# Kernel optimization log

Hardware: AMD Instinct MI355X
Metric: run time of the kernel (lower is better)

Reference implementation:

```python
import jax, jax.numpy as jnp
import numpy as np


def setup_inputs() -> dict:
    key = jax.random.key(0)
    ks = jax.random.split(key, 7)
    B, T, IN_F = 16384, 64, 48
    F = 32          # feature_size = len(INTERACTIVE_LIST)
    H = 128         # embedding_hidden_size
    TF, TH = T * F, T * H
    scale1 = 1.0 / np.sqrt(TF)
    scale2 = 1.0 / np.sqrt(TH)
    return {
        "x": jax.random.normal(ks[0], (B, T, IN_F), dtype=jnp.float32),
        "W1": jax.random.normal(ks[1], (TF, TH), dtype=jnp.float32) * scale1,
        "b1": jax.random.normal(ks[2], (TH,), dtype=jnp.float32) * scale1,
        "W2": jax.random.normal(ks[3], (TH, TF), dtype=jnp.float32) * scale2,
        "b2": jax.random.normal(ks[4], (TF,), dtype=jnp.float32) * scale2,
        "weight": jax.random.normal(ks[5], (T, F), dtype=jnp.float32),
        "bias": jax.random.normal(ks[6], (F,), dtype=jnp.float32) * (1.0 / np.sqrt(T)),
        "sample_index": jnp.arange(F, dtype=jnp.int32),
    }


def reference(x, W1, b1, W2, b2, weight, bias, sample_index):
    # x: [B, T, IN_F]; gather interactive feature columns -> [B, T, F]
    B = x.shape[0]
    T, F = weight.shape
    xs = jnp.take(x, sample_index, axis=2)            # [B, T, F]
    # pass_linear=True path: MLP on flattened time*feature vector
    h = jax.nn.relu(xs.reshape(B, T * F) @ W1 + b1)   # [B, T*H]; dropout = identity (eval)
    out = (h @ W2 + b2).reshape(B, T, F)              # [B, T, F]
    # vectorized form of the per-sample loop: sum over time of elementwise mul
    emb = jnp.einsum("btf,tf->bf", out, weight) + bias  # [B, F]
    return emb
```

## Files before the change

### kernel.cpp

```cpp
#include <hip/hip_runtime.h>
#include <hip/hip_bf16.h>

#define BATCH 16384
#define TT    64
#define INF   48
#define FF    32
#define TFD   2048
#define THD   8192

typedef __attribute__((ext_vector_type(8))) short bf16x8;
typedef __attribute__((ext_vector_type(4))) short bf16x4;
typedef __attribute__((ext_vector_type(4))) short short4v;
typedef __attribute__((ext_vector_type(4))) float f32x4;

#define SCHED __builtin_amdgcn_sched_barrier(0)
#define VMW(n) asm volatile("s_waitcnt vmcnt(" #n ")" ::: "memory")

__device__ inline void gload_lds16(const void* g, void* l) {
  __builtin_amdgcn_global_load_lds((const __attribute__((address_space(1))) void*)g,
                                   (__attribute__((address_space(3))) void*)l, 16, 0, 0);
}

__device__ inline f32x4 mfma16x16x16_bf16(bf16x4 a, bf16x4 b, f32x4 c) {
#if __has_builtin(__builtin_amdgcn_mfma_f32_16x16x16bf16_1k)
  return __builtin_amdgcn_mfma_f32_16x16x16bf16_1k(a, b, c, 0, 0, 0);
#else
  asm("v_mfma_f32_16x16x16_bf16 %0, %1, %2, %0" : "+v"(c) : "v"(a), "v"(b));
  return c;
#endif
}

__device__ inline short f32_to_bf16_bits(float x) {
  __hip_bfloat16 h = __float2bfloat16(x);
  return *reinterpret_cast<short*>(&h);
}


__global__ void gather_cast_frag(const float* __restrict__ x, const int* __restrict__ sidx,
                                 __hip_bfloat16* __restrict__ xsf) {
  __shared__ int sx[FF];
  if (threadIdx.x < FF) sx[threadIdx.x] = sidx[threadIdx.x];
  __syncthreads();
  const int b64 = blockIdx.x >> 2;
  const int tq  = blockIdx.x & 3;
  for (int it = 0; it < 16; ++it) {
    const int slot = (tq * 16 + it) * 256 + threadIdx.x;
    const int t  = slot >> 8;
    const int bi = (slot >> 6) & 3;
    const int l  = slot & 63;
    const int lo = l & 15, hi = l >> 4;
    const int row = b64 * 64 + bi * 16 + lo;
    const float* rp = x + ((size_t)row * TT + t) * INF;
    bf16x8 v;
    #pragma unroll
    for (int j = 0; j < 8; ++j) v[j] = f32_to_bf16_bits(rp[sx[hi * 8 + j]]);
    *(bf16x8*)(xsf + ((size_t)b64 * 16384 + slot) * 8) = v;
  }
}

__global__ void transpose_w1(const float* __restrict__ W1, __hip_bfloat16* __restrict__ W1t) {
  __shared__ float tile[64][65];
  const int k0 = blockIdx.x * 64;
  const int n0 = blockIdx.y * 64;
  const int tx = threadIdx.x & 63, ty = threadIdx.x >> 6;
  for (int r = ty; r < 64; r += 4)
    tile[r][tx] = W1[(size_t)(k0 + r) * THD + n0 + tx];
  __syncthreads();
  const int rn = threadIdx.x >> 4;
  const int kq = (threadIdx.x & 15) * 4;
  for (int rr = rn; rr < 64; rr += 16) {
    short4v v;
    #pragma unroll
    for (int i = 0; i < 4; ++i) v[i] = f32_to_bf16_bits(tile[kq + i][rr]);
    *(short4v*)(W1t + (size_t)(n0 + rr) * TFD + k0 + kq) = v;
  }
}

__global__ void make_w2eff(const float* __restrict__ W2, const float* __restrict__ b2,
                           const float* __restrict__ weight, const float* __restrict__ bias,
                           __hip_bfloat16* __restrict__ w2t, float* __restrict__ beff) {
  const int n = blockIdx.x * 8 + (threadIdx.x >> 5);
  const int f = threadIdx.x & 31;
  const float* wr = W2 + (size_t)n * TFD;
  float s = 0.f;
  #pragma unroll 8
  for (int t = 0; t < TT; ++t) s += wr[t * FF + f] * weight[t * FF + f];
  w2t[(size_t)f * THD + n] = __float2bfloat16(s);
  if (blockIdx.x == 0 && threadIdx.x < FF) {
    float sb = bias[f];
    for (int t = 0; t < TT; ++t) sb += b2[t * FF + f] * weight[t * FF + f];
    beff[f] = sb;
  }
}


__device__ inline void stage_w(char* buf, const __hip_bfloat16* __restrict__ w1t,
                               int n0, int k0, int wid, int l) {
  const int sub = l >> 3;
  const int c   = (l & 7) ^ sub;
  const int h   = c >> 2, kc = c & 3;
  const int r0  = wid * 8 + sub;
  const __hip_bfloat16* gw0 = w1t + (size_t)(n0 + 2 * r0 + h) * TFD + k0 + kc * 8;
  const __hip_bfloat16* gw1 = w1t + (size_t)(n0 + 128 + 2 * r0 + h) * TFD + k0 + kc * 8;
  char* lx = buf + wid * 1024;
  gload_lds16(gw0, lx);
  gload_lds16(gw1, lx + 8192);
}

__device__ __forceinline__ void k_iter(char* lds, int v, int strip,
    const char* __restrict__ xbase, const __hip_bfloat16* __restrict__ w1t,
    f32x4 (&acc)[8][4], bf16x8 (&xfu)[4],
    int wbase, int wid, int l, bool do_bar) {
  if (v <= 252) {
    const int vs = v + 3;
    stage_w(lds + (size_t)(vs & 7) * 16384, w1t,
            strip * 1024 + (vs >> 6) * 256, (vs & 63) * 32, wid, l);
  }
  SCHED;
  const char* buf = lds + (size_t)(v & 7) * 16384;
  bf16x8 w0  = *(const bf16x8*)(buf + wbase);
  bf16x8 w1f = *(const bf16x8*)(buf + wbase + 1024);
  #pragma unroll
  for (int g = 0; g < 4; ++g) {
    bf16x8 nw0, nw1;
    if (g < 3) {
      nw0 = *(const bf16x8*)(buf + wbase + (2 * g + 2) * 1024);
      nw1 = *(const bf16x8*)(buf + wbase + (2 * g + 3) * 1024);
    }
    __builtin_amdgcn_s_setprio(1);
    #pragma unroll
    for (int bi = 0; bi < 4; ++bi)
      acc[2 * g][bi] = __builtin_amdgcn_mfma_f32_16x16x32_bf16(w0, xfu[bi], acc[2 * g][bi], 0, 0, 0);
    #pragma unroll
    for (int bi = 0; bi < 4; ++bi)
      acc[2 * g + 1][bi] = __builtin_amdgcn_mfma_f32_16x16x32_bf16(w1f, xfu[bi], acc[2 * g + 1][bi], 0, 0, 0);
    __builtin_amdgcn_s_setprio(0);
    if (g < 3) { w0 = nw0; w1f = nw1; }
  }
  if (v <= 253) {
    const int u = (v + 2) & 63;
    #pragma unroll
    for (int bi = 0; bi < 4; ++bi)
      xfu[bi] = *(const bf16x8*)(xbase + (u * 4 + bi) * 1024);
  }
  SCHED;
  if (v <= 252)      { VMW(6); }
  else if (v == 253) { VMW(4); }
  else               { VMW(0); }
  SCHED;
  if (do_bar) {
    __builtin_amdgcn_s_barrier(); SCHED;
  }
}

__global__ __launch_bounds__(512, 2) void gemm_fused(
    const __hip_bfloat16* __restrict__ xsf,
    const __hip_bfloat16* __restrict__ w1t,
    const float* __restrict__ b1,
    const __hip_bfloat16* __restrict__ w2t,
    float* __restrict__ partial)
{
  __shared__ __align__(16) char lds[131072];
  const int tid = threadIdx.x;
  const int wid = tid >> 6, l = tid & 63;
  const int mq = wid >> 2, bq = wid & 3;
  const int lo = l & 15, hi = l >> 4;
  const int rl = lo >> 1;
  const int cofs = (((((lo & 1) << 2) | hi) ^ rl) << 4);
  const int strip = blockIdx.x & 7;
  const int bt = blockIdx.x >> 3;
  const int b0 = bt * 256;

  const int wbase = ((mq << 6) + rl) * 128 + cofs;
  const char* xbase = (const char*)xsf + ((size_t)(bt * 4 + bq) * 16384 + l) * 16;

  f32x4 acc2[2][4];
  #pragma unroll
  for (int fi = 0; fi < 2; ++fi)
    #pragma unroll
    for (int bi = 0; bi < 4; ++bi) { f32x4 z = {0.f,0.f,0.f,0.f}; acc2[fi][bi] = z; }

  f32x4 acc[8][4];
  #pragma unroll
  for (int mi = 0; mi < 8; ++mi)
    #pragma unroll
    for (int bi = 0; bi < 4; ++bi) { f32x4 z = {0.f,0.f,0.f,0.f}; acc[mi][bi] = z; }

  bf16x8 xfA[4], xfB[4];
  stage_w(lds, w1t, strip * 1024, 0, wid, l);
  SCHED;
  #pragma unroll
  for (int bi = 0; bi < 4; ++bi) xfA[bi] = *(const bf16x8*)(xbase + (0 * 4 + bi) * 1024);
  SCHED;
  stage_w(lds + 16384, w1t, strip * 1024, 32, wid, l);
  SCHED;
  #pragma unroll
  for (int bi = 0; bi < 4; ++bi) xfB[bi] = *(const bf16x8*)(xbase + (1 * 4 + bi) * 1024);
  SCHED;
  stage_w(lds + 32768, w1t, strip * 1024, 64, wid, l);
  SCHED;
  VMW(8); SCHED;
  __builtin_amdgcn_s_barrier(); SCHED;

  for (int vv = 0; vv < 256; vv += 2) {
    k_iter(lds, vv,     strip, xbase, w1t, acc, xfA, wbase, wid, l, false);
    k_iter(lds, vv + 1, strip, xbase, w1t, acc, xfB, wbase, wid, l, true);

    if ((vv & 63) == 62) {
      const int n0e = strip * 1024 + (vv >> 6) * 256;
      #pragma unroll
      for (int mi = 0; mi < 8; ++mi) {
        const int nbase = n0e + (mq << 7) + (mi << 4);
        const float4 b1v = *(const float4*)(b1 + nbase + (hi << 2));
        bf16x4 p[4];
        #pragma unroll
        for (int bi = 0; bi < 4; ++bi) {
          bf16x4 pk;
          #pragma unroll
          for (int j = 0; j < 4; ++j) {
            float v = acc[mi][bi][j] + ((const float*)&b1v)[j];
            v = v > 0.f ? v : 0.f;
            pk[j] = f32_to_bf16_bits(v);
          }
          p[bi] = pk;
        }
        bf16x4 a2[2];
        #pragma unroll
        for (int fi = 0; fi < 2; ++fi)
          a2[fi] = *(const bf16x4*)(w2t + (size_t)(fi * 16 + lo) * THD + nbase + (hi << 2));
        #pragma unroll
        for (int fi = 0; fi < 2; ++fi)
          #pragma unroll
          for (int bi = 0; bi < 4; ++bi)
            acc2[fi][bi] = mfma16x16x16_bf16(a2[fi], p[bi], acc2[fi][bi]);
        #pragma unroll
        for (int bi = 0; bi < 4; ++bi) { f32x4 z = {0.f,0.f,0.f,0.f}; acc[mi][bi] = z; }
      }
    }
  }

  float* sm = (float*)lds;
  __syncthreads();
  if (mq == 1) {
    #pragma unroll
    for (int fi = 0; fi < 2; ++fi)
      #pragma unroll
      for (int bi = 0; bi < 4; ++bi)
        *(f32x4*)(sm + ((bq << 6) + (bi << 4) + lo) * 32 + fi * 16 + (hi << 2)) = acc2[fi][bi];
  }
  __syncthreads();
  if (mq == 0) {
    #pragma unroll
    for (int fi = 0; fi < 2; ++fi)
      #pragma unroll
      for (int bi = 0; bi < 4; ++bi) {
        f32x4 other = *(const f32x4*)(sm + ((bq << 6) + (bi << 4) + lo) * 32 + fi * 16 + (hi << 2));
        f32x4 v = acc2[fi][bi] + other;
        *(f32x4*)(partial + ((size_t)strip * BATCH + b0 + (bq << 6) + (bi << 4) + lo) * FF + fi * 16 + (hi << 2)) = v;
      }
  }
}

__global__ void reduce_partial(const float* __restrict__ partial, const float* __restrict__ beff,
                               float* __restrict__ out) {
  const int idx = blockIdx.x * 256 + threadIdx.x;
  float s = beff[idx & 31];
  #pragma unroll
  for (int c = 0; c < 8; ++c) s += partial[(size_t)c * BATCH * FF + idx];
  out[idx] = s;
}


extern "C" void kernel_launch(void* const* d_in, const int* in_sizes, int n_in,
                              void* d_out, int out_size, void* d_ws, size_t ws_size,
                              hipStream_t stream) {
  const float* x      = (const float*)d_in[0];
  const float* W1     = (const float*)d_in[1];
  const float* b1     = (const float*)d_in[2];
  const float* W2     = (const float*)d_in[3];
  const float* b2     = (const float*)d_in[4];
  const float* weight = (const float*)d_in[5];
  const float* bias   = (const float*)d_in[6];
  const int*   sidx   = (const int*)d_in[7];

  char* ws = (char*)d_ws;
  __hip_bfloat16* xsf  = (__hip_bfloat16*)ws;
  __hip_bfloat16* w1t  = (__hip_bfloat16*)(ws + 67108864);
  __hip_bfloat16* w2t  = (__hip_bfloat16*)(ws + 100663296);
  float*          beff = (float*)(ws + 101187584);
  float*          part = (float*)(ws + 101188608);

  hipLaunchKernelGGL(gather_cast_frag, dim3(1024), dim3(256), 0, stream, x, sidx, xsf);
  hipLaunchKernelGGL(transpose_w1, dim3(32, 128), dim3(256), 0, stream, W1, w1t);
  hipLaunchKernelGGL(make_w2eff,   dim3(1024),    dim3(256), 0, stream, W2, b2, weight, bias, w2t, beff);
  hipLaunchKernelGGL(gemm_fused,   dim3(512),     dim3(512), 0, stream, xsf, w1t, b1, w2t, part);
  hipLaunchKernelGGL(reduce_partial, dim3(2048),  dim3(256), 0, stream, part, beff, (float*)d_out);
}
```

Before: 597.4 us.

## Switch fused GEMM to 32x32x16 MFMA tiles with matching fragment layouts

Replaces the 16x16x32 bf16 MFMA tiling in the main GEMM with 32x32x16 MFMAs. This changes the x fragment layout produced by the gather kernel, the LDS staging and swizzle of W1, and the accumulator shapes. The second GEMM now also uses 32x32 MFMAs, with a per-lane LDS exchange to rebuild the B fragment from the accumulator layout. The aim is fewer MFMA and LDS-read instructions per flop and higher MFMA throughput. The cost is extra LDS round trips and waits in the epilogue, and larger accumulator register tiles.

```diff
diff --git a/kernel.cpp b/kernel.cpp
--- a/kernel.cpp
+++ b/kernel.cpp
@@ -9,30 +9,31 @@
 #define THD   8192
 
 typedef __attribute__((ext_vector_type(8))) short bf16x8;
-typedef __attribute__((ext_vector_type(4))) short bf16x4;
 typedef __attribute__((ext_vector_type(4))) short short4v;
 typedef __attribute__((ext_vector_type(4))) float f32x4;
+typedef __attribute__((ext_vector_type(16))) float f32x16;
 
 #define SCHED __builtin_amdgcn_sched_barrier(0)
 #define VMW(n) asm volatile("s_waitcnt vmcnt(" #n ")" ::: "memory")
+#define LGKM0  asm volatile("s_waitcnt lgkmcnt(0)" ::: "memory")
 
 __device__ inline void gload_lds16(const void* g, void* l) {
   __builtin_amdgcn_global_load_lds((const __attribute__((address_space(1))) void*)g,
                                    (__attribute__((address_space(3))) void*)l, 16, 0, 0);
 }
 
-__device__ inline f32x4 mfma16x16x16_bf16(bf16x4 a, bf16x4 b, f32x4 c) {
-#if __has_builtin(__builtin_amdgcn_mfma_f32_16x16x16bf16_1k)
-  return __builtin_amdgcn_mfma_f32_16x16x16bf16_1k(a, b, c, 0, 0, 0);
-#else
-  asm("v_mfma_f32_16x16x16_bf16 %0, %1, %2, %0" : "+v"(c) : "v"(a), "v"(b));
-  return c;
-#endif
+__device__ inline f32x16 mfma32(bf16x8 a, bf16x8 b, f32x16 c) {
+  return __builtin_amdgcn_mfma_f32_32x32x16_bf16(a, b, c, 0, 0, 0);
 }
 
 __device__ inline short f32_to_bf16_bits(float x) {
   __hip_bfloat16 h = __float2bfloat16(x);
   return *reinterpret_cast<short*>(&h);
+}
+
+__device__ inline unsigned packbf(float a, float b) {
+  return ((unsigned)(unsigned short)f32_to_bf16_bits(b) << 16) |
+         (unsigned)(unsigned short)f32_to_bf16_bits(a);
 }
 
 
@@ -41,20 +42,19 @@
   __shared__ int sx[FF];
   if (threadIdx.x < FF) sx[threadIdx.x] = sidx[threadIdx.x];
   __syncthreads();
-  const int b64 = blockIdx.x >> 2;
-  const int tq  = blockIdx.x & 3;
-  for (int it = 0; it < 16; ++it) {
-    const int slot = (tq * 16 + it) * 256 + threadIdx.x;
-    const int t  = slot >> 8;
-    const int bi = (slot >> 6) & 3;
-    const int l  = slot & 63;
-    const int lo = l & 15, hi = l >> 4;
-    const int row = b64 * 64 + bi * 16 + lo;
-    const float* rp = x + ((size_t)row * TT + t) * INF;
+  const int g32 = blockIdx.x;
+  for (int it = 0; it < 32; ++it) {
+    const int slot = it * 256 + threadIdx.x;
+    const int u16 = slot >> 6;
+    const int l   = slot & 63;
+    const int lo  = l & 31, hi = l >> 5;
+    const int t   = u16 >> 1;
+    const int fb  = ((u16 & 1) << 4) + (hi << 3);
+    const float* rp = x + ((size_t)(g32 * 32 + lo) * TT + t) * INF;
     bf16x8 v;
     #pragma unroll
-    for (int j = 0; j < 8; ++j) v[j] = f32_to_bf16_bits(rp[sx[hi * 8 + j]]);
-    *(bf16x8*)(xsf + ((size_t)b64 * 16384 + slot) * 8) = v;
+    for (int j = 0; j < 8; ++j) v[j] = f32_to_bf16_bits(rp[sx[fb + j]]);
+    *(bf16x8*)(xsf + ((size_t)g32 * 8192 + slot) * 8) = v;
   }
 }
 
@@ -94,54 +94,49 @@
 }
 
 
-__device__ inline void stage_w(char* buf, const __hip_bfloat16* __restrict__ w1t,
-                               int n0, int k0, int wid, int l) {
-  const int sub = l >> 3;
-  const int c   = (l & 7) ^ sub;
-  const int h   = c >> 2, kc = c & 3;
-  const int r0  = wid * 8 + sub;
-  const __hip_bfloat16* gw0 = w1t + (size_t)(n0 + 2 * r0 + h) * TFD + k0 + kc * 8;
-  const __hip_bfloat16* gw1 = w1t + (size_t)(n0 + 128 + 2 * r0 + h) * TFD + k0 + kc * 8;
-  char* lx = buf + wid * 1024;
-  gload_lds16(gw0, lx);
-  gload_lds16(gw1, lx + 8192);
+__device__ inline void stage_w32(char* buf, const __hip_bfloat16* __restrict__ w1t,
+                                 int n0, int k0, int wid, int l) {
+  const int e = l >> 3;
+  const int p = l & 7;
+  #pragma unroll
+  for (int j = 0; j < 2; ++j) {
+    const int q  = j * 8 + e;
+    const int c  = q * 8 + (p ^ e);
+    const int R  = c >> 2, kc = c & 3;
+    const __hip_bfloat16* g = w1t + (size_t)(n0 + wid * 32 + R) * TFD + k0 + kc * 8;
+    gload_lds16(g, buf + wid * 2048 + j * 1024);
+  }
 }
 
 __device__ __forceinline__ void k_iter(char* lds, int v, int strip,
-    const char* __restrict__ xbase, const __hip_bfloat16* __restrict__ w1t,
-    f32x4 (&acc)[8][4], bf16x8 (&xfu)[4],
-    int wbase, int wid, int l, bool do_bar) {
+    const char* __restrict__ xb0, const char* __restrict__ xb1,
+    const __hip_bfloat16* __restrict__ w1t,
+    f32x16 (&acc)[4][2], bf16x8 (&xfu)[4],
+    int gbase, int rdo0, int rdo1, int wid, int l, bool do_bar) {
   if (v <= 252) {
     const int vs = v + 3;
-    stage_w(lds + (size_t)(vs & 7) * 16384, w1t,
-            strip * 1024 + (vs >> 6) * 256, (vs & 63) * 32, wid, l);
-  }
-  SCHED;
-  const char* buf = lds + (size_t)(v & 7) * 16384;
-  bf16x8 w0  = *(const bf16x8*)(buf + wbase);
-  bf16x8 w1f = *(const bf16x8*)(buf + wbase + 1024);
+    stage_w32(lds + (size_t)(vs & 7) * 16384, w1t,
+              strip * 1024 + (vs >> 6) * 256, (vs & 63) * 32, wid, l);
+  }
+  SCHED;
+  const char* buf = lds + (size_t)(v & 7) * 16384 + gbase;
   #pragma unroll
-  for (int g = 0; g < 4; ++g) {
-    bf16x8 nw0, nw1;
-    if (g < 3) {
-      nw0 = *(const bf16x8*)(buf + wbase + (2 * g + 2) * 1024);
-      nw1 = *(const bf16x8*)(buf + wbase + (2 * g + 3) * 1024);
-    }
+  for (int nt = 0; nt < 4; ++nt) {
+    const bf16x8 w0  = *(const bf16x8*)(buf + nt * 2048 + rdo0);
+    const bf16x8 w1f = *(const bf16x8*)(buf + nt * 2048 + rdo1);
     __builtin_amdgcn_s_setprio(1);
-    #pragma unroll
-    for (int bi = 0; bi < 4; ++bi)
-      acc[2 * g][bi] = __builtin_amdgcn_mfma_f32_16x16x32_bf16(w0, xfu[bi], acc[2 * g][bi], 0, 0, 0);
-    #pragma unroll
-    for (int bi = 0; bi < 4; ++bi)
-      acc[2 * g + 1][bi] = __builtin_amdgcn_mfma_f32_16x16x32_bf16(w1f, xfu[bi], acc[2 * g + 1][bi], 0, 0, 0);
+    acc[nt][0] = mfma32(w0,  xfu[0], acc[nt][0]);
+    acc[nt][0] = mfma32(w1f, xfu[1], acc[nt][0]);
+    acc[nt][1] = mfma32(w0,  xfu[2], acc[nt][1]);
+    acc[nt][1] = mfma32(w1f, xfu[3], acc[nt][1]);
     __builtin_amdgcn_s_setprio(0);
-    if (g < 3) { w0 = nw0; w1f = nw1; }
   }
   if (v <= 253) {
     const int u = (v + 2) & 63;
-    #pragma unroll
-    for (int bi = 0; bi < 4; ++bi)
-      xfu[bi] = *(const bf16x8*)(xbase + (u * 4 + bi) * 1024);
+    xfu[0] = *(const bf16x8*)(xb0 + (u * 2 + 0) * 1024);
+    xfu[1] = *(const bf16x8*)(xb0 + (u * 2 + 1) * 1024);
+    xfu[2] = *(const bf16x8*)(xb1 + (u * 2 + 0) * 1024);
+    xfu[3] = *(const bf16x8*)(xb1 + (u * 2 + 1) * 1024);
   }
   SCHED;
   if (v <= 252)      { VMW(6); }
@@ -164,77 +159,91 @@
   const int tid = threadIdx.x;
   const int wid = tid >> 6, l = tid & 63;
   const int mq = wid >> 2, bq = wid & 3;
-  const int lo = l & 15, hi = l >> 4;
-  const int rl = lo >> 1;
-  const int cofs = (((((lo & 1) << 2) | hi) ^ rl) << 4);
+  const int lo = l & 31, hi = l >> 5;
   const int strip = blockIdx.x & 7;
   const int bt = blockIdx.x >> 3;
   const int b0 = bt * 256;
 
-  const int wbase = ((mq << 6) + rl) * 128 + cofs;
-  const char* xbase = (const char*)xsf + ((size_t)(bt * 4 + bq) * 16384 + l) * 16;
-
-  f32x4 acc2[2][4];
+  int rdo0, rdo1;
+  {
+    const int c0 = (lo << 2) + hi;       const int q0 = c0 >> 3;
+    rdo0 = (q0 << 7) + ((((c0 & 7) ^ (q0 & 7))) << 4);
+    const int c1 = c0 + 2;               const int q1 = c1 >> 3;
+    rdo1 = (q1 << 7) + ((((c1 & 7) ^ (q1 & 7))) << 4);
+  }
+  const int gbase = mq << 13;
+
+  const char* xb0 = (const char*)xsf + (size_t)(bt * 8 + bq * 2) * 131072 + l * 16;
+  const char* xb1 = xb0 + 131072;
+
+  const f32x16 vzero = {0.f,0.f,0.f,0.f,0.f,0.f,0.f,0.f,0.f,0.f,0.f,0.f,0.f,0.f,0.f,0.f};
+
+  f32x16 acc2[2];
+  acc2[0] = vzero; acc2[1] = vzero;
+
+  f32x16 acc[4][2];
   #pragma unroll
-  for (int fi = 0; fi < 2; ++fi)
-    #pragma unroll
-    for (int bi = 0; bi < 4; ++bi) { f32x4 z = {0.f,0.f,0.f,0.f}; acc2[fi][bi] = z; }
-
-  f32x4 acc[8][4];
-  #pragma unroll
-  for (int mi = 0; mi < 8; ++mi)
-    #pragma unroll
-    for (int bi = 0; bi < 4; ++bi) { f32x4 z = {0.f,0.f,0.f,0.f}; acc[mi][bi] = z; }
+  for (int nt = 0; nt < 4; ++nt) { acc[nt][0] = vzero; acc[nt][1] = vzero; }
 
   bf16x8 xfA[4], xfB[4];
-  stage_w(lds, w1t, strip * 1024, 0, wid, l);
-  SCHED;
-  #pragma unroll
-  for (int bi = 0; bi < 4; ++bi) xfA[bi] = *(const bf16x8*)(xbase + (0 * 4 + bi) * 1024);
-  SCHED;
-  stage_w(lds + 16384, w1t, strip * 1024, 32, wid, l);
-  SCHED;
-  #pragma unroll
-  for (int bi = 0; bi < 4; ++bi) xfB[bi] = *(const bf16x8*)(xbase + (1 * 4 + bi) * 1024);
-  SCHED;
-  stage_w(lds + 32768, w1t, strip * 1024, 64, wid, l);
+  stage_w32(lds, w1t, strip * 1024, 0, wid, l);
+  SCHED;
+  xfA[0] = *(const bf16x8*)(xb0 + 0);    xfA[1] = *(const bf16x8*)(xb0 + 1024);
+  xfA[2] = *(const bf16x8*)(xb1 + 0);    xfA[3] = *(const bf16x8*)(xb1 + 1024);
+  SCHED;
+  stage_w32(lds + 16384, w1t, strip * 1024, 32, wid, l);
+  SCHED;
+  xfB[0] = *(const bf16x8*)(xb0 + 2048); xfB[1] = *(const bf16x8*)(xb0 + 3072);
+  xfB[2] = *(const bf16x8*)(xb1 + 2048); xfB[3] = *(const bf16x8*)(xb1 + 3072);
+  SCHED;
+  stage_w32(lds + 32768, w1t, strip * 1024, 64, wid, l);
   SCHED;
   VMW(8); SCHED;
   __builtin_amdgcn_s_barrier(); SCHED;
 
   for (int vv = 0; vv < 256; vv += 2) {
-    k_iter(lds, vv,     strip, xbase, w1t, acc, xfA, wbase, wid, l, false);
-    k_iter(lds, vv + 1, strip, xbase, w1t, acc, xfB, wbase, wid, l, true);
+    k_iter(lds, vv,     strip, xb0, xb1, w1t, acc, xfA, gbase, rdo0, rdo1, wid, l, false);
+    k_iter(lds, vv + 1, strip, xb0, xb1, w1t, acc, xfB, gbase, rdo0, rdo1, wid, l, true);
 
     if ((vv & 63) == 62) {
       const int n0e = strip * 1024 + (vv >> 6) * 256;
+      char* scr        = lds + 3 * 16384 + wid * 2048 + l * 16;
+      const char* pscr = lds + 3 * 16384 + wid * 2048 + ((l ^ 32) * 16) + (hi ? 8 : 0);
       #pragma unroll
-      for (int mi = 0; mi < 8; ++mi) {
-        const int nbase = n0e + (mq << 7) + (mi << 4);
-        const float4 b1v = *(const float4*)(b1 + nbase + (hi << 2));
-        bf16x4 p[4];
+      for (int nt = 0; nt < 4; ++nt) {
+        const int nb = n0e + (mq << 7) + (nt << 5);
         #pragma unroll
-        for (int bi = 0; bi < 4; ++bi) {
-          bf16x4 pk;
+        for (int hh = 0; hh < 2; ++hh) {
+          const bf16x8 af = *(const bf16x8*)(w2t + (size_t)lo * THD + nb + hh * 16 + (hi << 3));
+          const float4 bv0 = *(const float4*)(b1 + nb + hh * 16 + (hi << 2));
+          const float4 bv1 = *(const float4*)(b1 + nb + hh * 16 + 8 + (hi << 2));
           #pragma unroll
-          for (int j = 0; j < 4; ++j) {
-            float v = acc[mi][bi][j] + ((const float*)&b1v)[j];
-            v = v > 0.f ? v : 0.f;
-            pk[j] = f32_to_bf16_bits(v);
+          for (int btl = 0; btl < 2; ++btl) {
+            float r0 = acc[nt][btl][hh * 8 + 0] + bv0.x; r0 = r0 > 0.f ? r0 : 0.f;
+            float r1 = acc[nt][btl][hh * 8 + 1] + bv0.y; r1 = r1 > 0.f ? r1 : 0.f;
+            float r2 = acc[nt][btl][hh * 8 + 2] + bv0.z; r2 = r2 > 0.f ? r2 : 0.f;
+            float r3 = acc[nt][btl][hh * 8 + 3] + bv0.w; r3 = r3 > 0.f ? r3 : 0.f;
+            float r4 = acc[nt][btl][hh * 8 + 4] + bv1.x; r4 = r4 > 0.f ? r4 : 0.f;
+            float r5 = acc[nt][btl][hh * 8 + 5] + bv1.y; r5 = r5 > 0.f ? r5 : 0.f;
+            float r6 = acc[nt][btl][hh * 8 + 6] + bv1.z; r6 = r6 > 0.f ? r6 : 0.f;
+            float r7 = acc[nt][btl][hh * 8 + 7] + bv1.w; r7 = r7 > 0.f ? r7 : 0.f;
+            const unsigned a0 = packbf(r0, r1), a1 = packbf(r2, r3);
+            const unsigned c0 = packbf(r4, r5), c1 = packbf(r6, r7);
+            uint4 own; own.x = a0; own.y = a1; own.z = c0; own.w = c1;
+            SCHED;
+            *(uint4*)scr = own;
+            LGKM0; SCHED;
+            const uint2 pw = *(const uint2*)pscr;
+            LGKM0; SCHED;
+            uint4 fr;
+            if (hi == 0) { fr.x = a0;   fr.y = a1;   fr.z = pw.x; fr.w = pw.y; }
+            else         { fr.x = pw.x; fr.y = pw.y; fr.z = c0;   fr.w = c1;   }
+            const bf16x8 hf = *reinterpret_cast<const bf16x8*>(&fr);
+            acc2[btl] = mfma32(af, hf, acc2[btl]);
+            SCHED;
           }
-          p[bi] = pk;
         }
-        bf16x4 a2[2];
-        #pragma unroll
-        for (int fi = 0; fi < 2; ++fi)
-          a2[fi] = *(const bf16x4*)(w2t + (size_t)(fi * 16 + lo) * THD + nbase + (hi << 2));
-        #pragma unroll
-        for (int fi = 0; fi < 2; ++fi)
-          #pragma unroll
-          for (int bi = 0; bi < 4; ++bi)
-            acc2[fi][bi] = mfma16x16x16_bf16(a2[fi], p[bi], acc2[fi][bi]);
-        #pragma unroll
-        for (int bi = 0; bi < 4; ++bi) { f32x4 z = {0.f,0.f,0.f,0.f}; acc[mi][bi] = z; }
+        acc[nt][0] = vzero; acc[nt][1] = vzero;
       }
     }
   }
@@ -243,21 +252,29 @@
   __syncthreads();
   if (mq == 1) {
     #pragma unroll
-    for (int fi = 0; fi < 2; ++fi)
+    for (int btl = 0; btl < 2; ++btl) {
+      const int row = (bq << 6) + (btl << 5) + lo;
       #pragma unroll
-      for (int bi = 0; bi < 4; ++bi)
-        *(f32x4*)(sm + ((bq << 6) + (bi << 4) + lo) * 32 + fi * 16 + (hi << 2)) = acc2[fi][bi];
+      for (int q = 0; q < 4; ++q) {
+        f32x4 qv = { acc2[btl][q * 4 + 0], acc2[btl][q * 4 + 1],
+                     acc2[btl][q * 4 + 2], acc2[btl][q * 4 + 3] };
+        *(f32x4*)(sm + row * 32 + (q << 3) + (hi << 2)) = qv;
+      }
+    }
   }
   __syncthreads();
   if (mq == 0) {
     #pragma unroll
-    for (int fi = 0; fi < 2; ++fi)
+    for (int btl = 0; btl < 2; ++btl) {
+      const int row = (bq << 6) + (btl << 5) + lo;
       #pragma unroll
-      for (int bi = 0; bi < 4; ++bi) {
-        f32x4 other = *(const f32x4*)(sm + ((bq << 6) + (bi << 4) + lo) * 32 + fi * 16 + (hi << 2));
-        f32x4 v = acc2[fi][bi] + other;
-        *(f32x4*)(partial + ((size_t)strip * BATCH + b0 + (bq << 6) + (bi << 4) + lo) * FF + fi * 16 + (hi << 2)) = v;
+      for (int q = 0; q < 4; ++q) {
+        f32x4 qv = { acc2[btl][q * 4 + 0], acc2[btl][q * 4 + 1],
+                     acc2[btl][q * 4 + 2], acc2[btl][q * 4 + 3] };
+        qv = qv + *(const f32x4*)(sm + row * 32 + (q << 3) + (hi << 2));
+        *(f32x4*)(partial + ((size_t)strip * BATCH + b0 + row) * FF + (q << 3) + (hi << 2)) = qv;
       }
+    }
   }
 }
 
@@ -290,7 +307,7 @@
   float*          beff = (float*)(ws + 101187584);
   float*          part = (float*)(ws + 101188608);
 
-  hipLaunchKernelGGL(gather_cast_frag, dim3(1024), dim3(256), 0, stream, x, sidx, xsf);
+  hipLaunchKernelGGL(gather_cast_frag, dim3(512), dim3(256), 0, stream, x, sidx, xsf);
   hipLaunchKernelGGL(transpose_w1, dim3(32, 128), dim3(256), 0, stream, W1, w1t);
   hipLaunchKernelGGL(make_w2eff,   dim3(1024),    dim3(256), 0, stream, W2, b2, weight, bias, w2t, beff);
   hipLaunchKernelGGL(gemm_fused,   dim3(512),     dim3(512), 0, stream, xsf, w1t, b1, w2t, part);
```

New measurement: 663.9 us. +11.1%, slower.
